# Performance work log

Hardware: AMD Instinct MI355X
Metric: run time of the kernel (lower is better)

## Reference

```python
import jax, jax.numpy as jnp
import numpy as np

B, T = 64, 512
NTOKEN, NINP, NLAB, NHID, NCLASS = 50000, 256, 64, 512, 10


def _fq_signed(x, bits=8):
    # symmetric per-tensor int fake-quant with STE (Brevitas Int8*PerTensor style)
    qmax = float(2 ** (bits - 1) - 1)
    s = jnp.maximum(jnp.max(jnp.abs(x)), 1e-8) / qmax
    q = jnp.clip(jnp.round(x / s), -qmax - 1.0, qmax) * s
    return x + jax.lax.stop_gradient(q - x)


def _fq_unsigned(x, bits=8):
    # unsigned per-tensor fake-quant for sigmoid outputs (Uint8ActPerTensor)
    qmax = float(2 ** bits - 1)
    s = jnp.maximum(jnp.max(x), 1e-8) / qmax
    q = jnp.clip(jnp.round(x / s), 0.0, qmax) * s
    return x + jax.lax.stop_gradient(q - x)


def setup_inputs() -> dict:
    key = jax.random.key(0)
    ks = jax.random.split(key, 10)
    x = jax.random.randint(ks[0], (B, T), 0, NTOKEN)
    x_pred = jax.random.randint(ks[1], (B,), 0, NTOKEN)
    y_ext = jax.random.randint(ks[2], (B,), 0, NCLASS)
    initrange = 0.1
    emb_tok = jax.random.uniform(ks[3], (NTOKEN, NINP), minval=-initrange, maxval=initrange)
    emb_lab = jax.random.uniform(ks[4], (NCLASS, NLAB), minval=-initrange, maxval=initrange)
    din = NINP + NLAB
    k = 1.0 / np.sqrt(NHID)
    Wi = jax.random.uniform(ks[5], (4 * NHID, din), minval=-k, maxval=k)
    Wh = jax.random.uniform(ks[6], (4 * NHID, NHID), minval=-k, maxval=k)
    bi = jax.random.uniform(ks[7], (4 * NHID,), minval=-k, maxval=k)
    bh = jax.random.uniform(ks[8], (4 * NHID,), minval=-k, maxval=k)
    Wdec = jax.random.uniform(ks[9], (NTOKEN, NHID), minval=-initrange, maxval=initrange)
    return {"x": x, "x_pred": x_pred, "y_ext": y_ext, "emb_tok": emb_tok,
            "emb_lab": emb_lab, "Wi": Wi, "Wh": Wh, "bi": bi, "bh": bh, "Wdec": Wdec}


def _forward(x, x_pred, y_ext, emb_tok, emb_lab, Wi, Wh, bi, bh, Wdec):
    # quantized embeddings
    tok = _fq_signed(emb_tok)[x]                     # [B,T,NINP]
    lab = _fq_signed(emb_lab)[y_ext]                 # [B,NLAB]
    lab_t = jnp.broadcast_to(lab[:, None, :], (x.shape[0], x.shape[1], lab.shape[-1]))
    # concat_label='input': label embedding concatenated on feature dim, io-quantized
    inp = _fq_signed(jnp.concatenate([tok, lab_t], axis=-1))   # [B,T,NINP+NLAB]
    Wi_q, Wh_q = _fq_signed(Wi), _fq_signed(Wh)
    bias = bi + bh
    # precompute input contribution to all 4 gates
    xW = jnp.einsum('btd,gd->btg', inp, Wi_q) + bias  # [B,T,4H]
    H = Wh.shape[1]

    def step(carry, xw_t):
        h, c = carry
        gates = _fq_signed(xw_t + h @ Wh_q.T)        # gate-accumulator quant [B,4H]
        i_g, f_g, g_g, o_g = jnp.split(gates, 4, axis=-1)
        i = _fq_unsigned(jax.nn.sigmoid(i_g))
        f = _fq_unsigned(jax.nn.sigmoid(f_g))
        o = _fq_unsigned(jax.nn.sigmoid(o_g))
        g = _fq_signed(jnp.tanh(g_g))
        c = f * c + i * g
        h = _fq_signed(o * _fq_signed(jnp.tanh(c)))  # tanh quant then io quant
        return (h, c), h

    h0 = jnp.zeros((x.shape[0], H), inp.dtype)
    _, hs = jax.lax.scan(step, (h0, h0), jnp.swapaxes(xW, 0, 1))
    out_seq = jnp.swapaxes(hs, 0, 1)                 # [B,T,H]
    # (first + last hidden state) / 2
    result = (out_seq[:, 0, :] + out_seq[:, -1, :]) * 0.5
    logits = result @ _fq_signed(Wdec).T             # [B,NTOKEN]
    logp = jax.nn.log_softmax(logits, axis=-1)
    nll = -jnp.take_along_axis(logp, x_pred[:, None], axis=1)[:, 0]
    return jnp.mean(nll)                             # avg_loss=True


def reference(x, x_pred, y_ext, emb_tok, emb_lab, Wi, Wh, bi, bh, Wdec):
    return _forward(x, x_pred, y_ext, emb_tok, emb_lab, Wi, Wh, bi, bh, Wdec)
```

## Files before the change

kernel.cpp:

```cpp
#include <hip/hip_runtime.h>

typedef unsigned short u16;
typedef unsigned int u32;
typedef unsigned long long u64;
typedef short short8 __attribute__((ext_vector_type(8)));
typedef float f32x4 __attribute__((ext_vector_type(4)));

#define B_ 64
#define T_ 512
#define H_ 512
#define DIN_ 320
#define G4_ 2048
#define NTOK_ 50000
#define P_ 64

#define OFF_CTRL  0
#define OFF_FLAG1 1024
#define OFF_FLAG2 5120
#define OFF_FLAG3 9216
#define OFF_FLAG4 13312
#define OFF_NLL   17408
#define OFF_BIAS  17664
#define OFF_HBUF  26624
#define OFF_RESF  92160
#define OFF_WI8   223232
#define OFF_WH8   1533952
#define OFF_INP   3631104
#define OFF_LOG   24602624

__device__ inline u16 f2b_exact(float f) { return (u16)(__float_as_uint(f) >> 16); }
__device__ inline float fqv(float x, float s) { return fminf(fmaxf(rintf(x / s), -128.f), 127.f) * s; }
__device__ inline float sigm(float x) { return 1.f / (1.f + expf(-x)); }
__device__ inline float wredmax(float v) {
#pragma unroll
  for (int d = 1; d < 64; d <<= 1) v = fmaxf(v, __shfl_xor(v, d, 64));
  return v;
}
__device__ inline f32x4 MFMA(short8 a, short8 b, f32x4 c) {
  return __builtin_amdgcn_mfma_f32_16x16x32_bf16(a, b, c, 0, 0, 0);
}
__device__ inline float bredmax(float v, float* red) {
  int tid = threadIdx.x;
  red[tid] = v; __syncthreads();
  for (int s = 128; s > 0; s >>= 1) { if (tid < s) red[tid] = fmaxf(red[tid], red[tid + s]); __syncthreads(); }
  float r = red[0]; __syncthreads();
  return r;
}

__device__ inline void st_flag(u64* p, u64 v) {
  __hip_atomic_store(p, v, __ATOMIC_RELAXED, __HIP_MEMORY_SCOPE_AGENT);
}
__device__ inline u64 ld_flag(u64* p) {
  return __hip_atomic_load(p, __ATOMIC_RELAXED, __HIP_MEMORY_SCOPE_AGENT);
}
__device__ inline void st_h(u16* p, u16 v) {
  __hip_atomic_store(p, v, __ATOMIC_RELAXED, __HIP_MEMORY_SCOPE_AGENT);
}
__device__ inline u64 ld_h64(const u16* p) {
  return __hip_atomic_load((const u64*)p, __ATOMIC_RELAXED, __HIP_MEMORY_SCOPE_AGENT);
}

__global__ void kInit(u32* w32, u32* hbuf32) {
  int i = blockIdx.x * blockDim.x + threadIdx.x, st = gridDim.x * blockDim.x;
  for (int j = i; j < 4352; j += st) w32[j] = 0u;
  for (int j = i; j < B_ * H_ / 2; j += st) hbuf32[j] = 0u;
}

__global__ void kMaxAbs(const float* p, int n4, u32* slot) {
  __shared__ float red[256];
  int i0 = blockIdx.x * blockDim.x + threadIdx.x, st = gridDim.x * blockDim.x;
  float m = 0.f;
  const float4* p4 = (const float4*)p;
  for (int i = i0; i < n4; i += st) {
    float4 v = p4[i];
    m = fmaxf(fmaxf(m, fmaxf(fabsf(v.x), fabsf(v.y))), fmaxf(fabsf(v.z), fabsf(v.w)));
  }
  m = bredmax(m, red);
  if (threadIdx.x == 0) atomicMax(slot, __float_as_uint(m));
}

__global__ void kGatherMax(const int* x, const int* y, const float* emb_tok, const float* emb_lab, u32* ctrl) {
  __shared__ float red[256];
  int tid = threadIdx.x;
  float mt = 0.f, ml = 0.f;
  for (int p = blockIdx.x; p < B_ * T_; p += gridDim.x)
    mt = fmaxf(mt, fabsf(emb_tok[(size_t)x[p] * 256 + tid]));
  for (int p = blockIdx.x; p < B_; p += gridDim.x)
    if (tid < 64) ml = fmaxf(ml, fabsf(emb_lab[y[p] * 64 + tid]));
  float m = bredmax(mt, red);
  if (tid == 0) atomicMax(&ctrl[7], __float_as_uint(m));
  m = bredmax(ml, red);
  if (tid == 0) atomicMax(&ctrl[8], __float_as_uint(m));
}

__global__ void kScalars(u32* ctrl) {
  float* s = (float*)(ctrl + 16);
  float mt = __uint_as_float(ctrl[2]), ml = __uint_as_float(ctrl[3]);
  float mwi = __uint_as_float(ctrl[4]), mwh = __uint_as_float(ctrl[5]), mwd = __uint_as_float(ctrl[6]);
  float mtg = __uint_as_float(ctrl[7]), mlg = __uint_as_float(ctrl[8]);
  float s_tok = fmaxf(mt, 1e-8f) / 127.f, s_lab = fmaxf(ml, 1e-8f) / 127.f;
  s[0] = s_tok; s[1] = s_lab;
  s[2] = fmaxf(mwi, 1e-8f) / 127.f;
  s[3] = fmaxf(mwh, 1e-8f) / 127.f;
  s[4] = fmaxf(mwd, 1e-8f) / 127.f;
  float qt = fminf(rintf(mtg / s_tok), 127.f) * s_tok;
  float ql = fminf(rintf(mlg / s_lab), 127.f) * s_lab;
  s[5] = fmaxf(fmaxf(qt, ql), 1e-8f) / 127.f;
}

__global__ void kBuildInp(const int* x, const int* y, const float* emb_tok, const float* emb_lab,
                          const u32* ctrl, u16* inp) {
  const float* s = (const float*)(ctrl + 16);
  float s_tok = s[0], s_lab = s[1], s_inp = s[5];
  int p = blockIdx.x, b = p >> 9, t = p & 511, d = threadIdx.x;
  float v, s1;
  if (d < 256) { v = emb_tok[(size_t)x[p] * 256 + d]; s1 = s_tok; }
  else         { v = emb_lab[y[b] * 64 + (d - 256)];  s1 = s_lab; }
  float q1 = fminf(fmaxf(rintf(v / s1), -128.f), 127.f) * s1;
  float k2 = fminf(fmaxf(rintf(q1 / s_inp), -128.f), 127.f);
  inp[((size_t)t * B_ + b) * DIN_ + d] = f2b_exact(k2);
}

__global__ void kQuantW(const float* Wi, const float* Wh, const float* bi, const float* bh,
                        const u32* ctrl, u16* wi8, u16* wh8, float* biasF) {
  const float* s = (const float*)(ctrl + 16);
  float sWi = s[2], sWh = s[3];
  const int NA = G4_ * DIN_, NB = G4_ * H_;
  int i0 = blockIdx.x * blockDim.x + threadIdx.x, st = gridDim.x * blockDim.x;
  for (int i = i0; i < NA + NB + G4_; i += st) {
    if (i < NA) {
      wi8[i] = f2b_exact(fminf(fmaxf(rintf(Wi[i] / sWi), -128.f), 127.f));
    } else if (i < NA + NB) {
      int j = i - NA;
      wh8[j] = f2b_exact(fminf(fmaxf(rintf(Wh[j] / sWh), -128.f), 127.f));
    } else {
      int r = i - NA - NB;
      biasF[r] = bi[r] + bh[r];
    }
  }
}

__global__ __launch_bounds__(256, 1) void kScan(
    const u16* inp8, const u16* wi8, const u16* wh8, const float* biasF,
    const u32* ctrl, u64* flag1, u64* flag2, u64* flag3, u64* flag4,
    u16* hBuf, float* resF) {
  __shared__ u16 ldsWi[20 * 64 * 8];
  __shared__ u16 ldsWh[32 * 64 * 8];
  __shared__ float actT[32][66];
  __shared__ float biasT[32];
  __shared__ float sRed[4][8];
  __shared__ float bcast[8];

  const int tid = threadIdx.x, lane = tid & 63, wid = tid >> 6;
  const int quad = lane >> 4, l15 = lane & 15;
  const int blk = blockIdx.x, hb = blk * 8;
  const float* scal = (const float*)(ctrl + 16);
  const float sWi = scal[2], sWh = scal[3], s_inp = scal[5];
  const float sA = s_inp * sWi;

  for (int fid = wid; fid < 20; fid += 4) {
    int nt = fid / 10, ks = fid - nt * 10;
    int n = nt * 16 + l15, r = (n >> 3) * 512 + hb + (n & 7);
    *(uint4*)&ldsWi[(fid * 64 + lane) * 8] = *(const uint4*)(wi8 + (size_t)r * DIN_ + ks * 32 + quad * 8);
  }
  for (int fid = wid; fid < 32; fid += 4) {
    int nt = fid >> 4, ks = fid & 15;
    int n = nt * 16 + l15, r = (n >> 3) * 512 + hb + (n & 7);
    *(uint4*)&ldsWh[(fid * 64 + lane) * 8] = *(const uint4*)(wh8 + (size_t)r * H_ + ks * 32 + quad * 8);
  }
  if (tid < 32) { int r = (tid >> 3) * 512 + hb + (tid & 7); biasT[tid] = biasF[r]; }
  __syncthreads();

  const int m0 = wid * 16;
  const int jj0 = tid & 7, b0 = tid >> 3;
  const int jj1 = (tid + 256) & 7, b1 = (tid + 256) >> 3;
  float cReg[2] = {0.f, 0.f};
  float hFirst[2] = {0.f, 0.f};
  float s_h_prev = 1.0f;

  f32x4 nA0 = {0.f, 0.f, 0.f, 0.f}, nA1 = {0.f, 0.f, 0.f, 0.f};
  {
    const u16* ip = inp8 + ((size_t)(m0 + l15)) * DIN_ + quad * 8;
#pragma unroll
    for (int ks = 0; ks < 10; ++ks) {
      short8 a = *(const short8*)(ip + ks * 32);
      nA0 = MFMA(a, *(const short8*)&ldsWi[(ks * 64 + lane) * 8], nA0);
      nA1 = MFMA(a, *(const short8*)&ldsWi[((10 + ks) * 64 + lane) * 8], nA1);
    }
  }

  for (int t = 0; t < T_; ++t) {
    const u32 sq = (u32)(t * 4);
    f32x4 aA0 = nA0, aA1 = nA1;

    if (t > 0) {
      if (wid == 0) {
        u64* f4 = flag4 + lane * 8;
        for (;;) {
          u64 v = ld_flag(f4);
          if ((u32)(v >> 32) == sq) break;
          __builtin_amdgcn_s_sleep(2);
        }
      }
      __syncthreads();
      __builtin_amdgcn_sched_barrier(0);
    }

    f32x4 aB0 = {0.f,0.f,0.f,0.f}, aB1 = {0.f,0.f,0.f,0.f};
    const u16* hp = hBuf + (size_t)(m0 + l15) * H_ + quad * 8;
#pragma unroll
    for (int ks = 0; ks < 16; ++ks) {
      u64 w0 = ld_h64(hp + ks * 32);
      u64 w1 = ld_h64(hp + ks * 32 + 4);
      short8 a;
      ((u64*)&a)[0] = w0;
      ((u64*)&a)[1] = w1;
      aB0 = MFMA(a, *(const short8*)&ldsWh[(ks * 64 + lane) * 8], aB0);
      aB1 = MFMA(a, *(const short8*)&ldsWh[((16 + ks) * 64 + lane) * 8], aB1);
    }
    const float sB_ = s_h_prev * sWh;
    float vabs = 0.f, v0mx = -3e38f, v1mx = -3e38f, v1mn = 3e38f;
#pragma unroll
    for (int reg = 0; reg < 4; ++reg) {
      int m = m0 + quad * 4 + reg;
      float p0 = biasT[l15] + sA * aA0[reg] + sB_ * aB0[reg];
      float p1 = biasT[16 + l15] + sA * aA1[reg] + sB_ * aB1[reg];
      actT[l15][m] = p0; actT[16 + l15][m] = p1;
      vabs = fmaxf(vabs, fmaxf(fabsf(p0), fabsf(p1)));
      v0mx = fmaxf(v0mx, p0);
      v1mx = fmaxf(v1mx, p1);
      v1mn = fminf(v1mn, p1);
    }
    bool lo = (l15 < 8);
    float q[6];
    q[0] = vabs;
    q[1] = lo ? v0mx : -3e38f;
    q[2] = lo ? -3e38f : v0mx;
    q[3] = lo ? -3e38f : v1mx;
    q[4] = lo ? v1mx : -3e38f;
    q[5] = lo ? -v1mn : -3e38f;
#pragma unroll
    for (int d = 1; d < 64; d <<= 1) {
#pragma unroll
      for (int k = 0; k < 6; ++k) q[k] = fmaxf(q[k], __shfl_xor(q[k], d, 64));
    }
    if (lane == 0) {
#pragma unroll
      for (int k = 0; k < 6; ++k) sRed[wid][k] = q[k];
    }
    __syncthreads();
    if (tid < 6) {
      float m = fmaxf(fmaxf(sRed[0][tid], sRed[1][tid]), fmaxf(sRed[2][tid], sRed[3][tid]));
      st_flag(flag1 + blk * 8 + tid, (((u64)(sq + 1)) << 32) | (u64)__float_as_uint(m));
    }
    if (wid == 0) {
      u64 a0, a1, a2, a3, a4, a5;
      u64* fb = flag1 + lane * 8;
      const u32 e = sq + 1;
      for (;;) {
        a0 = ld_flag(fb + 0); a1 = ld_flag(fb + 1); a2 = ld_flag(fb + 2);
        a3 = ld_flag(fb + 3); a4 = ld_flag(fb + 4); a5 = ld_flag(fb + 5);
        if ((u32)(a0 >> 32) == e && (u32)(a1 >> 32) == e && (u32)(a2 >> 32) == e &&
            (u32)(a3 >> 32) == e && (u32)(a4 >> 32) == e && (u32)(a5 >> 32) == e) break;
        __builtin_amdgcn_s_sleep(2);
      }
      float g0 = __uint_as_float((u32)a0), g1 = __uint_as_float((u32)a1),
            g2 = __uint_as_float((u32)a2), g3 = __uint_as_float((u32)a3),
            g4 = __uint_as_float((u32)a4), g5 = __uint_as_float((u32)a5);
#pragma unroll
      for (int d = 1; d < 64; d <<= 1) {
        g0 = fmaxf(g0, __shfl_xor(g0, d, 64));
        g1 = fmaxf(g1, __shfl_xor(g1, d, 64));
        g2 = fmaxf(g2, __shfl_xor(g2, d, 64));
        g3 = fmaxf(g3, __shfl_xor(g3, d, 64));
        g4 = fmaxf(g4, __shfl_xor(g4, d, 64));
        g5 = fmaxf(g5, __shfl_xor(g5, d, 64));
      }
      if (lane == 0) {
        bcast[0] = g0; bcast[1] = g1; bcast[2] = g2;
        bcast[3] = g3; bcast[4] = g4; bcast[5] = g5;
      }
    }
    __syncthreads();
    const float s_g = fmaxf(bcast[0], 1e-8f) / 127.f;
    const float mi = bcast[1], mf = bcast[2], mo = bcast[3];
    const float mg = bcast[4], mgn = -bcast[5];
    const float s_i = fmaxf(sigm(fqv(mi, s_g)), 1e-8f) / 255.f;
    const float s_f = fmaxf(sigm(fqv(mf, s_g)), 1e-8f) / 255.f;
    const float s_o = fmaxf(sigm(fqv(mo, s_g)), 1e-8f) / 255.f;
    const float ga = fmaxf(fabsf(fqv(mg, s_g)), fabsf(fqv(mgn, s_g)));
    const float s_gt = fmaxf(tanhf(ga), 1e-8f) / 127.f;

    float oqv[2];
    {
      float vi = sigm(fqv(actT[jj0][b0], s_g));
      float vf = sigm(fqv(actT[8 + jj0][b0], s_g));
      float vg = tanhf(fqv(actT[16 + jj0][b0], s_g));
      float vo = sigm(fqv(actT[24 + jj0][b0], s_g));
      float iq = fminf(fmaxf(rintf(vi / s_i), 0.f), 255.f) * s_i;
      float fq = fminf(fmaxf(rintf(vf / s_f), 0.f), 255.f) * s_f;
      float gq = fminf(fmaxf(rintf(vg / s_gt), -128.f), 127.f) * s_gt;
      oqv[0] = fminf(fmaxf(rintf(vo / s_o), 0.f), 255.f) * s_o;
      cReg[0] = fq * cReg[0] + iq * gq;
      vi = sigm(fqv(actT[jj1][b1], s_g));
      vf = sigm(fqv(actT[8 + jj1][b1], s_g));
      vg = tanhf(fqv(actT[16 + jj1][b1], s_g));
      vo = sigm(fqv(actT[24 + jj1][b1], s_g));
      iq = fminf(fmaxf(rintf(vi / s_i), 0.f), 255.f) * s_i;
      fq = fminf(fmaxf(rintf(vf / s_f), 0.f), 255.f) * s_f;
      gq = fminf(fmaxf(rintf(vg / s_gt), -128.f), 127.f) * s_gt;
      oqv[1] = fminf(fmaxf(rintf(vo / s_o), 0.f), 255.f) * s_o;
      cReg[1] = fq * cReg[1] + iq * gq;
    }
    float lm = wredmax(fmaxf(fabsf(cReg[0]), fabsf(cReg[1])));
    if (lane == 0) sRed[wid][0] = lm;
    __syncthreads();
    if (tid == 0) {
      float m = fmaxf(fmaxf(sRed[0][0], sRed[1][0]), fmaxf(sRed[2][0], sRed[3][0]));
      st_flag(flag2 + blk * 8, (((u64)(sq + 2)) << 32) | (u64)__float_as_uint(m));
    }
    if (wid == 0) {
      u64* f2 = flag2 + lane * 8;
      u64 v;
      for (;;) {
        v = ld_flag(f2);
        if ((u32)(v >> 32) == sq + 2) break;
        __builtin_amdgcn_s_sleep(2);
      }
      float mc = __uint_as_float((u32)v);
#pragma unroll
      for (int d = 1; d < 64; d <<= 1) mc = fmaxf(mc, __shfl_xor(mc, d, 64));
      if (lane == 0) bcast[6] = mc;
    }
    __syncthreads();
    const float maxc = bcast[6];
    const float s_t = fmaxf(tanhf(maxc), 1e-8f) / 127.f;

    float hpv[2];
    hpv[0] = oqv[0] * fqv(tanhf(cReg[0]), s_t);
    hpv[1] = oqv[1] * fqv(tanhf(cReg[1]), s_t);
    lm = wredmax(fmaxf(fabsf(hpv[0]), fabsf(hpv[1])));
    if (lane == 0) sRed[wid][0] = lm;
    __syncthreads();
    if (tid == 0) {
      float m = fmaxf(fmaxf(sRed[0][0], sRed[1][0]), fmaxf(sRed[2][0], sRed[3][0]));
      st_flag(flag3 + blk * 8, (((u64)(sq + 3)) << 32) | (u64)__float_as_uint(m));
    }
    if (wid == 0) {
      u64* f3 = flag3 + lane * 8;
      u64 v;
      for (;;) {
        v = ld_flag(f3);
        if ((u32)(v >> 32) == sq + 3) break;
        __builtin_amdgcn_s_sleep(2);
      }
      float mh = __uint_as_float((u32)v);
#pragma unroll
      for (int d = 1; d < 64; d <<= 1) mh = fmaxf(mh, __shfl_xor(mh, d, 64));
      if (lane == 0) bcast[7] = mh;
    }
    __syncthreads();
    const float s_h = fmaxf(bcast[7], 1e-8f) / 127.f;

    {
      float hi = fminf(fmaxf(rintf(hpv[0] / s_h), -128.f), 127.f);
      st_h(hBuf + b0 * H_ + hb + jj0, f2b_exact(hi));
      float hv = hi * s_h;
      if (t == 0) hFirst[0] = hv;
      if (t == T_ - 1) resF[b0 * H_ + hb + jj0] = 0.5f * (hFirst[0] + hv);
      hi = fminf(fmaxf(rintf(hpv[1] / s_h), -128.f), 127.f);
      st_h(hBuf + b1 * H_ + hb + jj1, f2b_exact(hi));
      hv = hi * s_h;
      if (t == 0) hFirst[1] = hv;
      if (t == T_ - 1) resF[b1 * H_ + hb + jj1] = 0.5f * (hFirst[1] + hv);
    }
    s_h_prev = s_h;
    if (t < T_ - 1) {
      __syncthreads();
      if (tid == 0) st_flag(flag4 + blk * 8, (((u64)(sq + 4)) << 32) | 1u);
      nA0 = (f32x4){0.f, 0.f, 0.f, 0.f};
      nA1 = (f32x4){0.f, 0.f, 0.f, 0.f};
      const u16* ip = inp8 + ((size_t)(t + 1) * B_ + m0 + l15) * DIN_ + quad * 8;
#pragma unroll
      for (int ks = 0; ks < 10; ++ks) {
        short8 a = *(const short8*)(ip + ks * 32);
        nA0 = MFMA(a, *(const short8*)&ldsWi[(ks * 64 + lane) * 8], nA0);
        nA1 = MFMA(a, *(const short8*)&ldsWi[((10 + ks) * 64 + lane) * 8], nA1);
      }
    }
  }
}

__global__ __launch_bounds__(256) void kDecode(const float* resF, const float* Wdec,
                                               const u32* ctrl, float* logits) {
  const float sWd = ((const float*)(ctrl + 16))[4];
  int c = blockIdx.x * 256 + threadIdx.x;
  if (c >= NTOK_) return;
  const float4* wrow = (const float4*)(Wdec + (size_t)c * H_);
  float acc[64];
#pragma unroll
  for (int rr = 0; rr < 64; rr++) acc[rr] = 0.f;
  for (int k4 = 0; k4 < H_ / 4; k4++) {
    float4 w = wrow[k4];
    float w0 = fminf(fmaxf(rintf(w.x / sWd), -128.f), 127.f) * sWd;
    float w1 = fminf(fmaxf(rintf(w.y / sWd), -128.f), 127.f) * sWd;
    float w2 = fminf(fmaxf(rintf(w.z / sWd), -128.f), 127.f) * sWd;
    float w3 = fminf(fmaxf(rintf(w.w / sWd), -128.f), 127.f) * sWd;
    const float* rp = resF + k4 * 4;
#pragma unroll
    for (int rr = 0; rr < 64; rr++) {
      acc[rr] += rp[rr * H_ + 0] * w0 + rp[rr * H_ + 1] * w1 +
                 rp[rr * H_ + 2] * w2 + rp[rr * H_ + 3] * w3;
    }
  }
#pragma unroll
  for (int rr = 0; rr < 64; rr++) logits[(size_t)rr * NTOK_ + c] = acc[rr];
}

__global__ void kLoss(const float* logits, const int* x_pred, float* nll) {
  __shared__ float red[256];
  int b = blockIdx.x, tid = threadIdx.x;
  const float* row = logits + (size_t)b * NTOK_;
  float m = -3e38f;
  for (int i = tid; i < NTOK_; i += 256) m = fmaxf(m, row[i]);
  m = bredmax(m, red);
  float s = 0.f;
  for (int i = tid; i < NTOK_; i += 256) s += expf(row[i] - m);
  red[tid] = s; __syncthreads();
  for (int st = 128; st > 0; st >>= 1) { if (tid < st) red[tid] += red[tid + st]; __syncthreads(); }
  if (tid == 0) nll[b] = m + logf(red[0]) - row[x_pred[b]];
}

__global__ void kFinal(const float* nll, float* out) {
  float s = 0.f;
  for (int i = 0; i < B_; i++) s += nll[i];
  out[0] = s / 64.f;
}

extern "C" void kernel_launch(void* const* d_in, const int* in_sizes, int n_in,
                              void* d_out, int out_size, void* d_ws, size_t ws_size,
                              hipStream_t stream) {
  const int* x      = (const int*)d_in[0];
  const int* x_pred = (const int*)d_in[1];
  const int* y_ext  = (const int*)d_in[2];
  const float* emb_tok = (const float*)d_in[3];
  const float* emb_lab = (const float*)d_in[4];
  const float* Wi   = (const float*)d_in[5];
  const float* Wh   = (const float*)d_in[6];
  const float* bi   = (const float*)d_in[7];
  const float* bh   = (const float*)d_in[8];
  const float* Wdec = (const float*)d_in[9];

  char* W = (char*)d_ws;
  u32* ctrl    = (u32*)(W + OFF_CTRL);
  u64* flag1   = (u64*)(W + OFF_FLAG1);
  u64* flag2   = (u64*)(W + OFF_FLAG2);
  u64* flag3   = (u64*)(W + OFF_FLAG3);
  u64* flag4   = (u64*)(W + OFF_FLAG4);
  float* nll   = (float*)(W + OFF_NLL);
  float* biasF = (float*)(W + OFF_BIAS);
  u16* hBuf    = (u16*)(W + OFF_HBUF);
  float* resF  = (float*)(W + OFF_RESF);
  u16* wi8     = (u16*)(W + OFF_WI8);
  u16* wh8     = (u16*)(W + OFF_WH8);
  u16* inp     = (u16*)(W + OFF_INP);
  float* logits = (float*)(W + OFF_LOG);

  kInit<<<128, 256, 0, stream>>>(ctrl, (u32*)hBuf);
  kMaxAbs<<<1024, 256, 0, stream>>>(emb_tok, NTOK_ * 256 / 4, ctrl + 2);
  kMaxAbs<<<1, 256, 0, stream>>>(emb_lab, 10 * 64 / 4, ctrl + 3);
  kMaxAbs<<<320, 256, 0, stream>>>(Wi, G4_ * DIN_ / 4, ctrl + 4);
  kMaxAbs<<<512, 256, 0, stream>>>(Wh, G4_ * H_ / 4, ctrl + 5);
  kMaxAbs<<<1024, 256, 0, stream>>>(Wdec, NTOK_ * H_ / 4, ctrl + 6);
  kGatherMax<<<256, 256, 0, stream>>>(x, y_ext, emb_tok, emb_lab, ctrl);
  kScalars<<<1, 1, 0, stream>>>(ctrl);
  kBuildInp<<<B_ * T_, DIN_, 0, stream>>>(x, y_ext, emb_tok, emb_lab, ctrl, inp);
  kQuantW<<<4096, 256, 0, stream>>>(Wi, Wh, bi, bh, ctrl, wi8, wh8, biasF);

  kScan<<<P_, 256, 0, stream>>>(inp, wi8, wh8, biasF, ctrl, flag1, flag2, flag3, flag4, hBuf, resF);

  kDecode<<<(NTOK_ + 255) / 256, 256, 0, stream>>>(resF, Wdec, ctrl, logits);
  kLoss<<<B_, 256, 0, stream>>>(logits, x_pred, nll);
  kFinal<<<1, 1, 0, stream>>>(nll, (float*)d_out);
}
```

Measured before the change: 7.544 ms.

## Halve scan workgroups to 32 with 512 threads each; split decode K across halves

The persistent LSTM scan now uses 32 workgroups of 8 waves, each owning 16 hidden units instead of 8. Cross-block flag polling per step touches half as many peers, which cuts the latency of the three global max-reductions and the hidden-state barrier on every timestep. Per-block LDS weight storage and per-step MFMA work double in exchange. The decode kernel also splits the K dimension across two 256-thread halves and sums them through shared memory, at the cost of 64 extra barriers per block. tanh(c) is also computed before the reduction wait.

```diff
diff --git a/kernel.cpp b/kernel.cpp
--- a/kernel.cpp
+++ b/kernel.cpp
@@ -12,7 +12,7 @@
 #define DIN_ 320
 #define G4_ 2048
 #define NTOK_ 50000
-#define P_ 64
+#define P_ 32
 
 #define OFF_CTRL  0
 #define OFF_FLAG1 1024
@@ -140,40 +140,44 @@
   }
 }
 
-__global__ __launch_bounds__(256, 1) void kScan(
+__global__ __launch_bounds__(512, 1) void kScan(
     const u16* inp8, const u16* wi8, const u16* wh8, const float* biasF,
     const u32* ctrl, u64* flag1, u64* flag2, u64* flag3, u64* flag4,
     u16* hBuf, float* resF) {
-  __shared__ u16 ldsWi[20 * 64 * 8];
-  __shared__ u16 ldsWh[32 * 64 * 8];
-  __shared__ float actT[32][66];
-  __shared__ float biasT[32];
-  __shared__ float sRed[4][8];
+  __shared__ u16 ldsWi[40 * 64 * 8];
+  __shared__ u16 ldsWh[64 * 64 * 8];
+  __shared__ float actT[64][66];
+  __shared__ float biasT[64];
+  __shared__ float sRed[8][8];
   __shared__ float bcast[8];
 
   const int tid = threadIdx.x, lane = tid & 63, wid = tid >> 6;
   const int quad = lane >> 4, l15 = lane & 15;
-  const int blk = blockIdx.x, hb = blk * 8;
+  const int blk = blockIdx.x, hb = blk * 16;
+  const int bt = wid & 3, nh = wid >> 2;
   const float* scal = (const float*)(ctrl + 16);
   const float sWi = scal[2], sWh = scal[3], s_inp = scal[5];
   const float sA = s_inp * sWi;
 
-  for (int fid = wid; fid < 20; fid += 4) {
+  for (int fid = wid; fid < 40; fid += 8) {
     int nt = fid / 10, ks = fid - nt * 10;
-    int n = nt * 16 + l15, r = (n >> 3) * 512 + hb + (n & 7);
+    int n = nt * 16 + l15, r = (n >> 4) * 512 + hb + (n & 15);
     *(uint4*)&ldsWi[(fid * 64 + lane) * 8] = *(const uint4*)(wi8 + (size_t)r * DIN_ + ks * 32 + quad * 8);
   }
-  for (int fid = wid; fid < 32; fid += 4) {
+  for (int fid = wid; fid < 64; fid += 8) {
     int nt = fid >> 4, ks = fid & 15;
-    int n = nt * 16 + l15, r = (n >> 3) * 512 + hb + (n & 7);
+    int n = nt * 16 + l15, r = (n >> 4) * 512 + hb + (n & 15);
     *(uint4*)&ldsWh[(fid * 64 + lane) * 8] = *(const uint4*)(wh8 + (size_t)r * H_ + ks * 32 + quad * 8);
   }
-  if (tid < 32) { int r = (tid >> 3) * 512 + hb + (tid & 7); biasT[tid] = biasF[r]; }
+  if (tid < 64) { int r = (tid >> 4) * 512 + hb + (tid & 15); biasT[tid] = biasF[r]; }
   __syncthreads();
 
-  const int m0 = wid * 16;
-  const int jj0 = tid & 7, b0 = tid >> 3;
-  const int jj1 = (tid + 256) & 7, b1 = (tid + 256) >> 3;
+  const int m0 = bt * 16;
+  const int fA0 = (nh * 2) * 10, fA1 = (nh * 2 + 1) * 10;
+  const int fB0 = (nh * 2) * 16, fB1 = (nh * 2 + 1) * 16;
+  const int n0 = nh * 32 + l15, n1 = nh * 32 + 16 + l15;
+  const int jj0 = tid & 15, b0 = tid >> 4;
+  const int b1 = b0 + 32;
   float cReg[2] = {0.f, 0.f};
   float hFirst[2] = {0.f, 0.f};
   float s_h_prev = 1.0f;
@@ -184,8 +188,8 @@
 #pragma unroll
     for (int ks = 0; ks < 10; ++ks) {
       short8 a = *(const short8*)(ip + ks * 32);
-      nA0 = MFMA(a, *(const short8*)&ldsWi[(ks * 64 + lane) * 8], nA0);
-      nA1 = MFMA(a, *(const short8*)&ldsWi[((10 + ks) * 64 + lane) * 8], nA1);
+      nA0 = MFMA(a, *(const short8*)&ldsWi[((fA0 + ks) * 64 + lane) * 8], nA0);
+      nA1 = MFMA(a, *(const short8*)&ldsWi[((fA1 + ks) * 64 + lane) * 8], nA1);
     }
   }
 
@@ -195,7 +199,7 @@
 
     if (t > 0) {
       if (wid == 0) {
-        u64* f4 = flag4 + lane * 8;
+        u64* f4 = flag4 + (lane & 31) * 8;
         for (;;) {
           u64 v = ld_flag(f4);
           if ((u32)(v >> 32) == sq) break;
@@ -215,30 +219,29 @@
       short8 a;
       ((u64*)&a)[0] = w0;
       ((u64*)&a)[1] = w1;
-      aB0 = MFMA(a, *(const short8*)&ldsWh[(ks * 64 + lane) * 8], aB0);
-      aB1 = MFMA(a, *(const short8*)&ldsWh[((16 + ks) * 64 + lane) * 8], aB1);
+      aB0 = MFMA(a, *(const short8*)&ldsWh[((fB0 + ks) * 64 + lane) * 8], aB0);
+      aB1 = MFMA(a, *(const short8*)&ldsWh[((fB1 + ks) * 64 + lane) * 8], aB1);
     }
     const float sB_ = s_h_prev * sWh;
-    float vabs = 0.f, v0mx = -3e38f, v1mx = -3e38f, v1mn = 3e38f;
+    float vabs = 0.f, v0mx = -3e38f, v1mx = -3e38f, v0mn = 3e38f;
 #pragma unroll
     for (int reg = 0; reg < 4; ++reg) {
       int m = m0 + quad * 4 + reg;
-      float p0 = biasT[l15] + sA * aA0[reg] + sB_ * aB0[reg];
-      float p1 = biasT[16 + l15] + sA * aA1[reg] + sB_ * aB1[reg];
-      actT[l15][m] = p0; actT[16 + l15][m] = p1;
+      float p0 = biasT[n0] + sA * aA0[reg] + sB_ * aB0[reg];
+      float p1 = biasT[n1] + sA * aA1[reg] + sB_ * aB1[reg];
+      actT[n0][m] = p0; actT[n1][m] = p1;
       vabs = fmaxf(vabs, fmaxf(fabsf(p0), fabsf(p1)));
       v0mx = fmaxf(v0mx, p0);
       v1mx = fmaxf(v1mx, p1);
-      v1mn = fminf(v1mn, p1);
-    }
-    bool lo = (l15 < 8);
+      v0mn = fminf(v0mn, p0);
+    }
     float q[6];
     q[0] = vabs;
-    q[1] = lo ? v0mx : -3e38f;
-    q[2] = lo ? -3e38f : v0mx;
-    q[3] = lo ? -3e38f : v1mx;
-    q[4] = lo ? v1mx : -3e38f;
-    q[5] = lo ? -v1mn : -3e38f;
+    q[1] = (nh == 0) ? v0mx : -3e38f;
+    q[2] = (nh == 0) ? v1mx : -3e38f;
+    q[3] = (nh == 1) ? v1mx : -3e38f;
+    q[4] = (nh == 1) ? v0mx : -3e38f;
+    q[5] = (nh == 1) ? -v0mn : -3e38f;
 #pragma unroll
     for (int d = 1; d < 64; d <<= 1) {
 #pragma unroll
@@ -250,12 +253,13 @@
     }
     __syncthreads();
     if (tid < 6) {
-      float m = fmaxf(fmaxf(sRed[0][tid], sRed[1][tid]), fmaxf(sRed[2][tid], sRed[3][tid]));
+      float m = fmaxf(fmaxf(fmaxf(sRed[0][tid], sRed[1][tid]), fmaxf(sRed[2][tid], sRed[3][tid])),
+                      fmaxf(fmaxf(sRed[4][tid], sRed[5][tid]), fmaxf(sRed[6][tid], sRed[7][tid])));
       st_flag(flag1 + blk * 8 + tid, (((u64)(sq + 1)) << 32) | (u64)__float_as_uint(m));
     }
     if (wid == 0) {
       u64 a0, a1, a2, a3, a4, a5;
-      u64* fb = flag1 + lane * 8;
+      u64* fb = flag1 + (lane & 31) * 8;
       const u32 e = sq + 1;
       for (;;) {
         a0 = ld_flag(fb + 0); a1 = ld_flag(fb + 1); a2 = ld_flag(fb + 2);
@@ -294,33 +298,36 @@
     float oqv[2];
     {
       float vi = sigm(fqv(actT[jj0][b0], s_g));
-      float vf = sigm(fqv(actT[8 + jj0][b0], s_g));
-      float vg = tanhf(fqv(actT[16 + jj0][b0], s_g));
-      float vo = sigm(fqv(actT[24 + jj0][b0], s_g));
+      float vf = sigm(fqv(actT[16 + jj0][b0], s_g));
+      float vg = tanhf(fqv(actT[32 + jj0][b0], s_g));
+      float vo = sigm(fqv(actT[48 + jj0][b0], s_g));
       float iq = fminf(fmaxf(rintf(vi / s_i), 0.f), 255.f) * s_i;
       float fq = fminf(fmaxf(rintf(vf / s_f), 0.f), 255.f) * s_f;
       float gq = fminf(fmaxf(rintf(vg / s_gt), -128.f), 127.f) * s_gt;
       oqv[0] = fminf(fmaxf(rintf(vo / s_o), 0.f), 255.f) * s_o;
       cReg[0] = fq * cReg[0] + iq * gq;
-      vi = sigm(fqv(actT[jj1][b1], s_g));
-      vf = sigm(fqv(actT[8 + jj1][b1], s_g));
-      vg = tanhf(fqv(actT[16 + jj1][b1], s_g));
-      vo = sigm(fqv(actT[24 + jj1][b1], s_g));
+      vi = sigm(fqv(actT[jj0][b1], s_g));
+      vf = sigm(fqv(actT[16 + jj0][b1], s_g));
+      vg = tanhf(fqv(actT[32 + jj0][b1], s_g));
+      vo = sigm(fqv(actT[48 + jj0][b1], s_g));
       iq = fminf(fmaxf(rintf(vi / s_i), 0.f), 255.f) * s_i;
       fq = fminf(fmaxf(rintf(vf / s_f), 0.f), 255.f) * s_f;
       gq = fminf(fmaxf(rintf(vg / s_gt), -128.f), 127.f) * s_gt;
       oqv[1] = fminf(fmaxf(rintf(vo / s_o), 0.f), 255.f) * s_o;
       cReg[1] = fq * cReg[1] + iq * gq;
     }
+    float tc0 = tanhf(cReg[0]);
+    float tc1 = tanhf(cReg[1]);
     float lm = wredmax(fmaxf(fabsf(cReg[0]), fabsf(cReg[1])));
     if (lane == 0) sRed[wid][0] = lm;
     __syncthreads();
     if (tid == 0) {
-      float m = fmaxf(fmaxf(sRed[0][0], sRed[1][0]), fmaxf(sRed[2][0], sRed[3][0]));
+      float m = fmaxf(fmaxf(fmaxf(sRed[0][0], sRed[1][0]), fmaxf(sRed[2][0], sRed[3][0])),
+                      fmaxf(fmaxf(sRed[4][0], sRed[5][0]), fmaxf(sRed[6][0], sRed[7][0])));
       st_flag(flag2 + blk * 8, (((u64)(sq + 2)) << 32) | (u64)__float_as_uint(m));
     }
     if (wid == 0) {
-      u64* f2 = flag2 + lane * 8;
+      u64* f2 = flag2 + (lane & 31) * 8;
       u64 v;
       for (;;) {
         v = ld_flag(f2);
@@ -337,17 +344,18 @@
     const float s_t = fmaxf(tanhf(maxc), 1e-8f) / 127.f;
 
     float hpv[2];
-    hpv[0] = oqv[0] * fqv(tanhf(cReg[0]), s_t);
-    hpv[1] = oqv[1] * fqv(tanhf(cReg[1]), s_t);
+    hpv[0] = oqv[0] * (fminf(fmaxf(rintf(tc0 / s_t), -128.f), 127.f) * s_t);
+    hpv[1] = oqv[1] * (fminf(fmaxf(rintf(tc1 / s_t), -128.f), 127.f) * s_t);
     lm = wredmax(fmaxf(fabsf(hpv[0]), fabsf(hpv[1])));
     if (lane == 0) sRed[wid][0] = lm;
     __syncthreads();
     if (tid == 0) {
-      float m = fmaxf(fmaxf(sRed[0][0], sRed[1][0]), fmaxf(sRed[2][0], sRed[3][0]));
+      float m = fmaxf(fmaxf(fmaxf(sRed[0][0], sRed[1][0]), fmaxf(sRed[2][0], sRed[3][0])),
+                      fmaxf(fmaxf(sRed[4][0], sRed[5][0]), fmaxf(sRed[6][0], sRed[7][0])));
       st_flag(flag3 + blk * 8, (((u64)(sq + 3)) << 32) | (u64)__float_as_uint(m));
     }
     if (wid == 0) {
-      u64* f3 = flag3 + lane * 8;
+      u64* f3 = flag3 + (lane & 31) * 8;
       u64 v;
       for (;;) {
         v = ld_flag(f3);
@@ -369,10 +377,10 @@
       if (t == 0) hFirst[0] = hv;
       if (t == T_ - 1) resF[b0 * H_ + hb + jj0] = 0.5f * (hFirst[0] + hv);
       hi = fminf(fmaxf(rintf(hpv[1] / s_h), -128.f), 127.f);
-      st_h(hBuf + b1 * H_ + hb + jj1, f2b_exact(hi));
+      st_h(hBuf + b1 * H_ + hb + jj0, f2b_exact(hi));
       hv = hi * s_h;
       if (t == 0) hFirst[1] = hv;
-      if (t == T_ - 1) resF[b1 * H_ + hb + jj1] = 0.5f * (hFirst[1] + hv);
+      if (t == T_ - 1) resF[b1 * H_ + hb + jj0] = 0.5f * (hFirst[1] + hv);
     }
     s_h_prev = s_h;
     if (t < T_ - 1) {
@@ -384,37 +392,47 @@
 #pragma unroll
       for (int ks = 0; ks < 10; ++ks) {
         short8 a = *(const short8*)(ip + ks * 32);
-        nA0 = MFMA(a, *(const short8*)&ldsWi[(ks * 64 + lane) * 8], nA0);
-        nA1 = MFMA(a, *(const short8*)&ldsWi[((10 + ks) * 64 + lane) * 8], nA1);
-      }
-    }
-  }
-}
-
-__global__ __launch_bounds__(256) void kDecode(const float* resF, const float* Wdec,
+        nA0 = MFMA(a, *(const short8*)&ldsWi[((fA0 + ks) * 64 + lane) * 8], nA0);
+        nA1 = MFMA(a, *(const short8*)&ldsWi[((fA1 + ks) * 64 + lane) * 8], nA1);
+      }
+    }
+  }
+}
+
+__global__ __launch_bounds__(512) void kDecode(const float* resF, const float* Wdec,
                                                const u32* ctrl, float* logits) {
+  __shared__ float shb[256];
   const float sWd = ((const float*)(ctrl + 16))[4];
-  int c = blockIdx.x * 256 + threadIdx.x;
-  if (c >= NTOK_) return;
-  const float4* wrow = (const float4*)(Wdec + (size_t)c * H_);
+  int half = threadIdx.x >> 8;
+  int lt = threadIdx.x & 255;
+  int c = blockIdx.x * 256 + lt;
+  bool act = (c < NTOK_);
   float acc[64];
 #pragma unroll
   for (int rr = 0; rr < 64; rr++) acc[rr] = 0.f;
-  for (int k4 = 0; k4 < H_ / 4; k4++) {
-    float4 w = wrow[k4];
-    float w0 = fminf(fmaxf(rintf(w.x / sWd), -128.f), 127.f) * sWd;
-    float w1 = fminf(fmaxf(rintf(w.y / sWd), -128.f), 127.f) * sWd;
-    float w2 = fminf(fmaxf(rintf(w.z / sWd), -128.f), 127.f) * sWd;
-    float w3 = fminf(fmaxf(rintf(w.w / sWd), -128.f), 127.f) * sWd;
-    const float* rp = resF + k4 * 4;
-#pragma unroll
-    for (int rr = 0; rr < 64; rr++) {
-      acc[rr] += rp[rr * H_ + 0] * w0 + rp[rr * H_ + 1] * w1 +
-                 rp[rr * H_ + 2] * w2 + rp[rr * H_ + 3] * w3;
-    }
-  }
-#pragma unroll
-  for (int rr = 0; rr < 64; rr++) logits[(size_t)rr * NTOK_ + c] = acc[rr];
+  if (act) {
+    const float4* wrow = (const float4*)(Wdec + (size_t)c * H_);
+    int k40 = half * 64;
+    for (int k4 = k40; k4 < k40 + 64; k4++) {
+      float4 w = wrow[k4];
+      float w0 = fminf(fmaxf(rintf(w.x / sWd), -128.f), 127.f) * sWd;
+      float w1 = fminf(fmaxf(rintf(w.y / sWd), -128.f), 127.f) * sWd;
+      float w2 = fminf(fmaxf(rintf(w.z / sWd), -128.f), 127.f) * sWd;
+      float w3 = fminf(fmaxf(rintf(w.w / sWd), -128.f), 127.f) * sWd;
+      const float* rp = resF + k4 * 4;
+#pragma unroll
+      for (int rr = 0; rr < 64; rr++) {
+        acc[rr] += rp[rr * H_ + 0] * w0 + rp[rr * H_ + 1] * w1 +
+                   rp[rr * H_ + 2] * w2 + rp[rr * H_ + 3] * w3;
+      }
+    }
+  }
+  for (int rr = 0; rr < 64; rr++) {
+    if (half) shb[lt] = acc[rr];
+    __syncthreads();
+    if (!half && act) logits[(size_t)rr * NTOK_ + c] = acc[rr] + shb[lt];
+    __syncthreads();
+  }
 }
 
 __global__ void kLoss(const float* logits, const int* x_pred, float* nll) {
@@ -477,9 +495,9 @@
   kBuildInp<<<B_ * T_, DIN_, 0, stream>>>(x, y_ext, emb_tok, emb_lab, ctrl, inp);
   kQuantW<<<4096, 256, 0, stream>>>(Wi, Wh, bi, bh, ctrl, wi8, wh8, biasF);
 
-  kScan<<<P_, 256, 0, stream>>>(inp, wi8, wh8, biasF, ctrl, flag1, flag2, flag3, flag4, hBuf, resF);
-
-  kDecode<<<(NTOK_ + 255) / 256, 256, 0, stream>>>(resF, Wdec, ctrl, logits);
+  kScan<<<P_, 512, 0, stream>>>(inp, wi8, wh8, biasF, ctrl, flag1, flag2, flag3, flag4, hBuf, resF);
+
+  kDecode<<<(NTOK_ + 255) / 256, 512, 0, stream>>>(resF, Wdec, ctrl, logits);
   kLoss<<<B_, 256, 0, stream>>>(logits, x_pred, nll);
   kFinal<<<1, 1, 0, stream>>>(nll, (float*)d_out);
 }
```

New measurement: 10.22 ms. +35.4%, slower.
